# Optimization experiments

Hardware: AMD Instinct MI355X
Metric: run time of the kernel (lower is better)

The kernel has to match this reference:

```python
import jax, jax.numpy as jnp
import numpy as np

N, E, D = 20000, 160000, 128   # nodes, edges, d_model
GH, HC = 4, 128                # TransformerConv heads, per-head channels (= out_channels)
MH = 4                         # temporal MHA heads
MC = D // MH                   # temporal MHA per-head dim
EPS = 1e-5


def layer_norm(x, g, b):
    mu = x.mean(-1, keepdims=True)
    var = ((x - mu) ** 2).mean(-1, keepdims=True)
    return (x - mu) * jax.lax.rsqrt(var + EPS) * g + b


def forward(x, temporal_encoding, gq_w, gq_b, gk_w, gk_b, gv_w, gv_b, gs_w, gs_b,
            mha_wq, mha_bq, mha_wk, mha_bk, mha_wv, mha_bv, mha_wo, mha_bo,
            ffn_w1, ffn_b1, ffn_w2, ffn_b2,
            ln1_g, ln1_b, ln2_g, ln2_b, ln3_g, ln3_b, edge_index):
    src, dst = edge_index[0], edge_index[1]
    n = x.shape[0]
    # --- TransformerConv(in=D, out=D, heads=GH, concat=False, root_weight=True) ---
    q = (x @ gq_w.T + gq_b).reshape(n, GH, HC)
    k = (x @ gk_w.T + gk_b).reshape(n, GH, HC)
    v = (x @ gv_w.T + gv_b).reshape(n, GH, HC)
    # per-edge attention logits: <q_i, k_j> / sqrt(out_channels), message j->i
    alpha = (q[dst] * k[src]).sum(-1) / jnp.sqrt(jnp.asarray(HC, x.dtype))  # [E, GH]
    # numerically-stable segment softmax over incoming edges of each dst node
    m = jax.ops.segment_max(alpha, dst, num_segments=n)                     # [N, GH]
    ex = jnp.exp(alpha - m[dst])
    den = jax.ops.segment_sum(ex, dst, num_segments=n)
    w = ex / den[dst]                                                       # [E, GH]
    agg = jax.ops.segment_sum(w[..., None] * v[src], dst, num_segments=n)  # [N, GH, HC]
    graph_out = agg.mean(1) + (x @ gs_w.T + gs_b)  # concat=False -> head mean; + root skip lin
    x1 = layer_norm(x + graph_out, ln1_g, ln1_b)   # dropout is identity at eval
    # --- temporal MHA: per-node query (len 1) attends to its temporal encoding (kv len 1) ---
    tq = (x1 @ mha_wq.T + mha_bq).reshape(n, MH, MC)
    tk = (temporal_encoding @ mha_wk.T + mha_bk).reshape(n, MH, MC)
    tv = (temporal_encoding @ mha_wv.T + mha_bv).reshape(n, MH, MC)
    scores = (tq * tk).sum(-1, keepdims=True) / jnp.sqrt(jnp.asarray(MC, x.dtype))  # [N, MH, 1]
    attn = jax.nn.softmax(scores, axis=-1)  # exactly ones (single kv position); kept for fidelity
    temp_out = (attn * tv).reshape(n, D) @ mha_wo.T + mha_bo
    x2 = layer_norm(x1 + temp_out, ln2_g, ln2_b)
    # --- FFN ---
    h = jax.nn.relu(x2 @ ffn_w1.T + ffn_b1)
    ffn_out = h @ ffn_w2.T + ffn_b2
    return layer_norm(x2 + ffn_out, ln3_g, ln3_b)


def setup_inputs() -> dict:
    ks = jax.random.split(jax.random.key(0), 16)
    s = 0.05
    def p(i, shape):
        return jax.random.normal(ks[i], shape, jnp.float32) * s
    z = lambda *sh: jnp.zeros(sh, jnp.float32)
    o = lambda *sh: jnp.ones(sh, jnp.float32)
    return {
        "x": p(0, (N, D)),
        "temporal_encoding": p(1, (N, D)),
        "gq_w": p(2, (GH * HC, D)), "gq_b": z(GH * HC),
        "gk_w": p(3, (GH * HC, D)), "gk_b": z(GH * HC),
        "gv_w": p(4, (GH * HC, D)), "gv_b": z(GH * HC),
        "gs_w": p(5, (D, D)), "gs_b": z(D),
        "mha_wq": p(6, (D, D)), "mha_bq": z(D),
        "mha_wk": p(7, (D, D)), "mha_bk": z(D),
        "mha_wv": p(8, (D, D)), "mha_bv": z(D),
        "mha_wo": p(9, (D, D)), "mha_bo": z(D),
        "ffn_w1": p(10, (4 * D, D)), "ffn_b1": z(4 * D),
        "ffn_w2": p(11, (D, 4 * D)), "ffn_b2": z(D),
        "ln1_g": o(D), "ln1_b": z(D),
        "ln2_g": o(D), "ln2_b": z(D),
        "ln3_g": o(D), "ln3_b": z(D),
        "edge_index": jax.random.randint(ks[12], (2, E), 0, N, jnp.int32),
    }


def reference(x, temporal_encoding, gq_w, gq_b, gk_w, gk_b, gv_w, gv_b, gs_w, gs_b,
              mha_wq, mha_bq, mha_wk, mha_bk, mha_wv, mha_bv, mha_wo, mha_bo,
              ffn_w1, ffn_b1, ffn_w2, ffn_b2,
              ln1_g, ln1_b, ln2_g, ln2_b, ln3_g, ln3_b, edge_index):
    return forward(x, temporal_encoding, gq_w, gq_b, gk_w, gk_b, gv_w, gv_b, gs_w, gs_b,
                   mha_wq, mha_bq, mha_wk, mha_bk, mha_wv, mha_bv, mha_wo, mha_bo,
                   ffn_w1, ffn_b1, ffn_w2, ffn_b2,
                   ln1_g, ln1_b, ln2_g, ln2_b, ln3_g, ln3_b, edge_index)
```

## Files before the change

### kernel.cpp

```cpp
#include <hip/hip_runtime.h>

#define NN 20000
#define EE 160000
#define DD 128
#define GHC 512
#define INV_SQRT_HC 0.08838834764831845f

typedef __attribute__((ext_vector_type(8))) short short8;
typedef __attribute__((ext_vector_type(4))) short short4v;
typedef __attribute__((ext_vector_type(4))) float float4v;
typedef __attribute__((ext_vector_type(2))) float float2v;
typedef __attribute__((ext_vector_type(4))) unsigned uint4v;
typedef __attribute__((ext_vector_type(2))) unsigned uint2v;

__device__ inline float bf2f(unsigned short u) {
    union { unsigned u; float f; } x; x.u = ((unsigned)u) << 16; return x.f;
}
__device__ inline unsigned short f2bf(float f) {
    union { float f; unsigned u; } x; x.f = f;
    unsigned u = x.u;
    unsigned r = (u + 0x7fffu + ((u >> 16) & 1u)) >> 16;
    return (unsigned short)r;
}

#if defined(__has_builtin)
#if __has_builtin(__builtin_amdgcn_cvt_pk_f32_fp8) && __has_builtin(__builtin_amdgcn_cvt_pk_fp8_f32)
#define HW_FP8 1
#endif
#endif
#ifndef HW_FP8
#define HW_FP8 0
#endif

#if !HW_FP8
__device__ inline unsigned char sw_enc_fp8(float f) {
    if (!(f == f)) return 0x7f;
    unsigned s = (f < 0.f) ? 0x80u : 0u;
    float a = fabsf(f);
    if (a >= 448.f) return (unsigned char)(s | 0x7e);
    if (a < 5.96046448e-8f) return (unsigned char)s;
    int e; frexpf(a, &e);
    int E = e - 1;
    if (E < -6) E = -6;
    float q = ldexpf(rintf(ldexpf(a, 3 - E)), E - 3);
    if (q == 0.f) return (unsigned char)s;
    union { float f; unsigned u; } x; x.f = q;
    int qe = (int)((x.u >> 23) & 0xff) - 127;
    if (qe < -6) {
        unsigned mant = (unsigned)rintf(ldexpf(q, 9));
        return (unsigned char)(s | mant);
    }
    unsigned mant = (x.u >> 20) & 7;
    int ebits = qe + 7;
    if (ebits > 15) { ebits = 15; mant = 6; }
    return (unsigned char)(s | ((unsigned)ebits << 3) | mant);
}
__device__ inline float sw_dec_fp8(unsigned char u) {
    unsigned s = u >> 7, e = (u >> 3) & 15, m = u & 7;
    float v = e ? ldexpf((float)(8 + m), (int)e - 10) : ldexpf((float)m, -9);
    return s ? -v : v;
}
#endif

__device__ inline unsigned short fp8_enc2(float a, float b) {
#if HW_FP8
    int r = __builtin_amdgcn_cvt_pk_fp8_f32(a, b, 0, false);
    return (unsigned short)(r & 0xffff);
#else
    return (unsigned short)(sw_enc_fp8(a) | ((unsigned)sw_enc_fp8(b) << 8));
#endif
}
__device__ inline float2v fp8_dec2_lo(unsigned w) {
#if HW_FP8
    return __builtin_amdgcn_cvt_pk_f32_fp8((int)w, false);
#else
    float2v r;
    r[0] = sw_dec_fp8((unsigned char)(w & 0xff));
    r[1] = sw_dec_fp8((unsigned char)((w >> 8) & 0xff));
    return r;
#endif
}
__device__ inline float2v fp8_dec2_hi(unsigned w) {
#if HW_FP8
    return __builtin_amdgcn_cvt_pk_f32_fp8((int)w, true);
#else
    float2v r;
    r[0] = sw_dec_fp8((unsigned char)((w >> 16) & 0xff));
    r[1] = sw_dec_fp8((unsigned char)(w >> 24));
    return r;
#endif
}

struct WPack { const void* in[18]; };
__device__ __constant__ const int WSZ[18] = {
    65536, 65536, 65536, 512, 512, 512,
    16384, 128, 65536, 512, 65536, 128,
    128, 128, 128, 128, 128, 128 };

__global__ void prep_kernel(const float* __restrict__ x, const float* __restrict__ te,
                            unsigned short* __restrict__ xcout, WPack p,
                            unsigned short* __restrict__ wcout,
                            const float* __restrict__ wv, const float* __restrict__ bv,
                            const float* __restrict__ wo, const float* __restrict__ bo,
                            unsigned short* __restrict__ wcomb,
                            unsigned short* __restrict__ bcomb,
                            const int* __restrict__ e_dst, int* __restrict__ counts)
{
    const int b = blockIdx.x;
    const int tid = threadIdx.x;
    if (b < 1024) {
        const long n4half = (long)NN * DD / 4;
        short4v* out4 = reinterpret_cast<short4v*>(xcout);
        long i = (long)b * 256 + tid;
        const long stride = 1024L * 256;
        const long tot = 2 * n4half;
        for (; i < tot; i += stride) {
            const float4v* src = (i < n4half)
                ? reinterpret_cast<const float4v*>(x)
                : reinterpret_cast<const float4v*>(te) - n4half;
            float4v v = src[i];
            short4v o;
            o[0] = (short)f2bf(v[0]); o[1] = (short)f2bf(v[1]);
            o[2] = (short)f2bf(v[2]); o[3] = (short)f2bf(v[3]);
            out4[i] = o;
        }
    } else if (b < 1600) {
        const int seg = (b - 1024) >> 5;
        const int rep = (b - 1024) & 31;
        int off = 0;
#pragma unroll
        for (int s = 0; s < 18; ++s) if (s < seg) off += WSZ[s];
        const int n = WSZ[seg];
        const float* q = (const float*)p.in[seg];
        for (int i = rep * 256 + tid; i < n; i += 32 * 256)
            wcout[off + i] = f2bf(q[i]);
    } else if (b < 1664) {
        int e = (b - 1600) * 256 + tid;
        int i = e >> 7, kk = e & 127;
        float s = 0.f;
        for (int j = 0; j < 128; ++j)
            s += wo[i * 128 + j] * wv[j * 128 + kk];
        wcomb[e] = f2bf(s);
        if (b == 1600 && tid < 128) {
            float t = 0.f;
            for (int j = 0; j < 128; ++j) t += wo[tid * 128 + j] * bv[j];
            bcomb[tid] = f2bf(t + bo[tid]);
        }
    } else {
        int e = (b - 1664) * 256 + tid;
        if (e < EE) {
            int d = e_dst[e];
            if (d >= 0 && d < NN) atomicAdd(&counts[d], 1);
        }
    }
}

__global__ __launch_bounds__(256) void gemm3_kernel(
    const unsigned short* __restrict__ A, const unsigned short* __restrict__ W,
    const unsigned short* __restrict__ bias, unsigned short* __restrict__ out,
    unsigned char* __restrict__ kvout, int M, int Nout, int split, int relu,
    int nxg, int ncol)
{
    __shared__ short8 wslab[2048];
    __shared__ __attribute__((aligned(16))) unsigned stile[4][16][36];
    const int tid  = threadIdx.x;
    const int lane = tid & 63;
    const int wid  = tid >> 6;
    const int quad = lane >> 4;
    const int l15  = lane & 15;

    const int nb  = nxg * ncol;
    const int qq  = nb >> 3, rm = nb & 7;
    const int xcd = blockIdx.x & 7, slot = blockIdx.x >> 3;
    const int c   = (xcd < rm) ? xcd * (qq + 1) + slot
                               : rm * (qq + 1) + (xcd - rm) * qq + slot;
    const int xg = c / ncol;
    const int yg = c - xg * ncol;
    const int colbase0 = yg * 128;
    const int rowg = xg * 256;

    const bool isfp8 = (colbase0 >= split);
    const int kvcol = colbase0 - split;
    const int which = isfp8 ? (kvcol >> 9) : 0;
    const int head  = isfp8 ? ((kvcol & 511) >> 7) : 0;

    const short8* A8 = reinterpret_cast<const short8*>(A);
    const short8* W8 = reinterpret_cast<const short8*>(W);

    short8 a4[4];
    {
        int arow = rowg + wid * 16 + l15;
        if (arow >= M) arow = M - 1;
#pragma unroll
        for (int i = 0; i < 4; ++i) a4[i] = A8[(size_t)arow * 16 + i * 4 + quad];
    }

#pragma unroll
    for (int rep = 0; rep < 8; ++rep) {
        int f   = rep * 256 + tid;
        int fl  = f & 63;
        int fi  = (f >> 6) & 3;
        int ft  = (f >> 8) & 3;
        int ftt = f >> 10;
        int wrow = colbase0 + ftt * 64 + 16 * ft + (fl & 15);
        wslab[f] = W8[(size_t)wrow * 16 + fi * 4 + (fl >> 4)];
    }

    float bvv[2][4];
#pragma unroll
    for (int tt = 0; tt < 2; ++tt)
#pragma unroll
        for (int t = 0; t < 4; ++t)
            bvv[tt][t] = bf2f(bias[colbase0 + tt * 64 + 16 * t + l15]);

    __syncthreads();

    unsigned short* fp = reinterpret_cast<unsigned short*>(&stile[wid][0][0]);

#pragma unroll
    for (int tg = 0; tg < 4; ++tg) {
        const int rowbase = rowg + tg * 64 + wid * 16;

        short8 a4n[4];
        if (tg < 3) {
            int arow = rowbase + 64 + l15;
            if (arow >= M) arow = M - 1;
#pragma unroll
            for (int i = 0; i < 4; ++i) a4n[i] = A8[(size_t)arow * 16 + i * 4 + quad];
        }

#pragma unroll
        for (int tt = 0; tt < 2; ++tt) {
            float4v acc[4];
#pragma unroll
            for (int t = 0; t < 4; ++t) acc[t] = (float4v){0.f, 0.f, 0.f, 0.f};

#pragma unroll
            for (int i = 0; i < 4; ++i) {
#pragma unroll
                for (int t = 0; t < 4; ++t) {
                    short8 b = wslab[((tt * 4 + t) * 4 + i) * 64 + lane];
                    acc[t] = __builtin_amdgcn_mfma_f32_16x16x32_bf16(a4[i], b, acc[t], 0, 0, 0);
                }
            }

            if (!isfp8) {
#pragma unroll
                for (int t = 0; t < 4; ++t) {
#pragma unroll
                    for (int r = 0; r < 4; ++r) {
                        float vv = acc[t][r] + bvv[tt][t];
                        if (relu) vv = fmaxf(vv, 0.f);
                        float ov = __shfl_xor(vv, 1, 64);
                        if ((l15 & 1) == 0)
                            stile[wid][quad * 4 + r][8 * t + (l15 >> 1)] =
                                (unsigned)f2bf(vv) | ((unsigned)f2bf(ov) << 16);
                    }
                }
                const int rr0 = lane >> 3;
                const int cd  = (lane & 7) * 4;
#pragma unroll
                for (int it = 0; it < 2; ++it) {
                    int rw = rr0 + it * 8;
                    int grow = rowbase + rw;
                    if (grow < M) {
                        uint4v v = *reinterpret_cast<const uint4v*>(&stile[wid][rw][cd]);
                        *reinterpret_cast<uint4v*>(&out[(size_t)grow * Nout + colbase0 + tt * 64 + cd * 2]) = v;
                    }
                }
            } else {
#pragma unroll
                for (int t = 0; t < 4; ++t) {
#pragma unroll
                    for (int r = 0; r < 4; ++r) {
                        float vv = (acc[t][r] + bvv[tt][t]) * 256.f;
                        float ov = __shfl_xor(vv, 1, 64);
                        if ((l15 & 1) == 0)
                            fp[(quad * 4 + r) * 72 + tt * 32 + ((16 * t + l15) >> 1)] =
                                fp8_enc2(vv, ov);
                    }
                }
            }
        }

        if (isfp8) {
#pragma unroll
            for (int it = 0; it < 2; ++it) {
                int u = lane + it * 64;
                int row = u >> 3;
                int part = u & 7;
                int grow = rowbase + row;
                if (grow < M) {
                    uint4v v = *reinterpret_cast<const uint4v*>(&fp[row * 72 + part * 8]);
                    size_t ro = (size_t)grow * 1024 + (size_t)which * 512
                              + (size_t)head * 128 + (size_t)part * 16;
                    *reinterpret_cast<uint4v*>(kvout + ro) = v;
                }
            }
        }

        if (tg < 3) {
#pragma unroll
            for (int i = 0; i < 4; ++i) a4[i] = a4n[i];
        }
    }
}

__global__ __launch_bounds__(256) void gemm_ln2_kernel(
    const unsigned short* __restrict__ A, const unsigned short* __restrict__ W,
    const unsigned short* __restrict__ bias,
    const float* __restrict__ residf, const float* __restrict__ c,
    const unsigned short* __restrict__ g, const unsigned short* __restrict__ beta,
    float* __restrict__ outf, unsigned short* __restrict__ outb, int M, int K)
{
    __shared__ short8 wslab[2048];
    __shared__ unsigned short stile[4][16][136];
    const int tid  = threadIdx.x;
    const int lane = tid & 63;
    const int wid  = tid >> 6;
    const int quad = lane >> 4;
    const int l15  = lane & 15;
    const int rowbase = blockIdx.x * 64 + wid * 16;

    int arow = rowbase + l15;
    if (arow >= M) arow = M - 1;

    const short8* A8 = reinterpret_cast<const short8*>(A);
    const short8* W8 = reinterpret_cast<const short8*>(W);
    const int k8 = K >> 3;
    const int kchunks = K >> 7;

    float4v acc[2][4];
#pragma unroll
    for (int tt = 0; tt < 2; ++tt)
#pragma unroll
        for (int t = 0; t < 4; ++t) acc[tt][t] = (float4v){0.f, 0.f, 0.f, 0.f};

    for (int cc = 0; cc < kchunks; ++cc) {
        if (cc > 0) __syncthreads();
#pragma unroll
        for (int rep = 0; rep < 8; ++rep) {
            int f   = rep * 256 + tid;
            int fl  = f & 63;
            int fi  = (f >> 6) & 3;
            int ft  = (f >> 8) & 3;
            int ftt = f >> 10;
            int wrow = ftt * 64 + 16 * ft + (fl & 15);
            wslab[f] = W8[(size_t)wrow * k8 + cc * 16 + fi * 4 + (fl >> 4)];
        }
        short8 a4[4];
#pragma unroll
        for (int i = 0; i < 4; ++i) a4[i] = A8[(size_t)arow * k8 + cc * 16 + i * 4 + quad];
        __syncthreads();
#pragma unroll
        for (int tt = 0; tt < 2; ++tt)
#pragma unroll
            for (int i = 0; i < 4; ++i)
#pragma unroll
                for (int t = 0; t < 4; ++t) {
                    short8 b = wslab[((tt * 4 + t) * 4 + i) * 64 + lane];
                    acc[tt][t] = __builtin_amdgcn_mfma_f32_16x16x32_bf16(a4[i], b, acc[tt][t], 0, 0, 0);
                }
    }

#pragma unroll
    for (int tt = 0; tt < 2; ++tt)
#pragma unroll
        for (int t = 0; t < 4; ++t) {
            float bv = bf2f(bias[tt * 64 + 16 * t + l15]);
#pragma unroll
            for (int r = 0; r < 4; ++r)
                stile[wid][quad * 4 + r][tt * 64 + 16 * t + l15] = f2bf(acc[tt][t][r] + bv);
        }

    const int r  = lane >> 2;
    const int p  = lane & 3;
    const int grow = rowbase + r;
    const int gr = (grow < M) ? grow : M - 1;

    float v[32];
    const short8* st8 = reinterpret_cast<const short8*>(&stile[wid][r][p * 32]);
#pragma unroll
    for (int q = 0; q < 4; ++q) {
        short8 sb = st8[q];
#pragma unroll
        for (int j = 0; j < 8; ++j) v[q * 8 + j] = bf2f((unsigned short)sb[j]);
    }
    const float4v* r4 = reinterpret_cast<const float4v*>(&residf[(size_t)gr * 128 + p * 32]);
#pragma unroll
    for (int q = 0; q < 8; ++q) {
        float4v rv = r4[q];
#pragma unroll
        for (int j = 0; j < 4; ++j) v[q * 4 + j] += rv[j];
    }
    if (c) {
        const float4v* c4 = reinterpret_cast<const float4v*>(&c[(size_t)gr * 128 + p * 32]);
#pragma unroll
        for (int q = 0; q < 8; ++q) {
            float4v cv = c4[q];
#pragma unroll
            for (int j = 0; j < 4; ++j) v[q * 4 + j] += cv[j];
        }
    }
    float s = 0.f, sq = 0.f;
#pragma unroll
    for (int i = 0; i < 32; ++i) { s += v[i]; sq += v[i] * v[i]; }
    s  += __shfl_xor(s, 1, 64);  s  += __shfl_xor(s, 2, 64);
    sq += __shfl_xor(sq, 1, 64); sq += __shfl_xor(sq, 2, 64);
    float mu  = s * (1.f / 128.f);
    float var = sq * (1.f / 128.f) - mu * mu;
    float rs  = rsqrtf(fmaxf(var, 0.f) + 1e-5f);

    if (grow < M) {
        const short8* g8 = reinterpret_cast<const short8*>(&g[p * 32]);
        const short8* b8 = reinterpret_cast<const short8*>(&beta[p * 32]);
        float o[32];
#pragma unroll
        for (int q = 0; q < 4; ++q) {
            short8 gg = g8[q], bb = b8[q];
#pragma unroll
            for (int j = 0; j < 8; ++j)
                o[q * 8 + j] = (v[q * 8 + j] - mu) * rs * bf2f((unsigned short)gg[j])
                               + bf2f((unsigned short)bb[j]);
        }
        float4v* o4 = reinterpret_cast<float4v*>(outf + (size_t)grow * 128 + p * 32);
#pragma unroll
        for (int q = 0; q < 8; ++q) {
            float4v ov = {o[q * 4], o[q * 4 + 1], o[q * 4 + 2], o[q * 4 + 3]};
            o4[q] = ov;
        }
        if (outb) {
            short8* ob8 = reinterpret_cast<short8*>(outb + (size_t)grow * 128 + p * 32);
#pragma unroll
            for (int q = 0; q < 4; ++q) {
                short8 oo;
#pragma unroll
                for (int j = 0; j < 8; ++j) oo[j] = (short)f2bf(o[q * 8 + j]);
                ob8[q] = oo;
            }
        }
    }
}

__global__ __launch_bounds__(1024) void scan_kernel(
    const int* __restrict__ counts, int* __restrict__ offsets, int* __restrict__ pos, int n)
{
    __shared__ int wsum[16];
    __shared__ int carry_s;
    const int tid = threadIdx.x;
    const int wid = tid >> 6, lane = tid & 63;
    int vals[20];
#pragma unroll
    for (int cI = 0; cI < 20; ++cI) {
        int i = cI * 1024 + tid;
        vals[cI] = (i < n) ? counts[i] : 0;
    }
    if (tid == 0) carry_s = 0;
    __syncthreads();
#pragma unroll
    for (int cI = 0; cI < 20; ++cI) {
        int i = cI * 1024 + tid;
        int val = vals[cI];
        int x = val;
#pragma unroll
        for (int off = 1; off < 64; off <<= 1) {
            int t = __shfl_up(x, off, 64);
            if (lane >= off) x += t;
        }
        if (lane == 63) wsum[wid] = x;
        __syncthreads();
        if (wid == 0 && lane < 16) {
            int s = wsum[lane];
#pragma unroll
            for (int off = 1; off < 16; off <<= 1) {
                int t = __shfl_up(s, off, 64);
                if (lane >= off) s += t;
            }
            wsum[lane] = s;
        }
        __syncthreads();
        int prefix = (wid > 0 ? wsum[wid - 1] : 0) + carry_s;
        int ex = prefix + x - val;
        if (i < n) { offsets[i] = ex; pos[i] = ex; }
        __syncthreads();
        if (tid == 0) carry_s += wsum[15];
        __syncthreads();
    }
    if (tid == 0) offsets[n] = carry_s;
}

__global__ void scatter_kernel(const int* __restrict__ src, const int* __restrict__ dst,
                               int* __restrict__ pos, int* __restrict__ sorted_src, int E)
{
    int e = blockIdx.x * 256 + threadIdx.x;
    if (e < E) {
        int d = dst[e];
        if (d >= 0 && d < NN) {
            int p = atomicAdd(&pos[d], 1);
            if (p >= 0 && p < E) sorted_src[p] = src[e];
        }
    }
}

__device__ inline void agg_edge(const uint2v& kk, const uint2v& vv,
                                const float* qf, float* acc, float& ssum)
{
    float2v k01 = fp8_dec2_lo(kk[0]);
    float2v k23 = fp8_dec2_hi(kk[0]);
    float2v k45 = fp8_dec2_lo(kk[1]);
    float2v k67 = fp8_dec2_hi(kk[1]);
    float dot = qf[0] * k01[0] + qf[1] * k01[1] + qf[2] * k23[0] + qf[3] * k23[1]
              + qf[4] * k45[0] + qf[5] * k45[1] + qf[6] * k67[0] + qf[7] * k67[1];
    dot += __shfl_xor(dot, 1, 64);
    dot += __shfl_xor(dot, 2, 64);
    dot += __shfl_xor(dot, 4, 64);
    dot += __shfl_xor(dot, 8, 64);
    float pp = __expf(dot);
    ssum += pp;
    float2v v01 = fp8_dec2_lo(vv[0]);
    float2v v23 = fp8_dec2_hi(vv[0]);
    float2v v45 = fp8_dec2_lo(vv[1]);
    float2v v67 = fp8_dec2_hi(vv[1]);
    acc[0] += pp * v01[0]; acc[1] += pp * v01[1];
    acc[2] += pp * v23[0]; acc[3] += pp * v23[1];
    acc[4] += pp * v45[0]; acc[5] += pp * v45[1];
    acc[6] += pp * v67[0]; acc[7] += pp * v67[1];
}

__global__ __launch_bounds__(256) void agg_kernel(
    const unsigned short* __restrict__ q, const unsigned char* __restrict__ kvb,
    const int* __restrict__ offsets, const int* __restrict__ srcs,
    float* __restrict__ aggb)
{
    __shared__ float sacc[4][64][8];
    __shared__ float sssum[4][64];
    const int tid  = threadIdx.x;
    const int wid  = tid >> 6;
    const int lane = tid & 63;
    const int node = blockIdx.x * 2 + (wid >> 1);
    const int half = wid & 1;

    const short8* q8 = reinterpret_cast<const short8*>(q);
    const int fidx = (lane >> 4) * 16 + (lane & 15);
    const int koff = fidx * 8;

    short8 qv = q8[(size_t)node * 64 + fidx];
    float qf[8];
#pragma unroll
    for (int i = 0; i < 8; ++i)
        qf[i] = bf2f((unsigned short)qv[i]) * (INV_SQRT_HC / 256.f);

    int beg = offsets[node], end = offsets[node + 1];
    if (beg < 0) beg = 0;
    if (end > EE) end = EE;
    float ssum = 0.f;
    float acc[8];
#pragma unroll
    for (int i = 0; i < 8; ++i) acc[i] = 0.f;

    const int start = beg + half;
    int nce = (end > start) ? ((end - start + 1) >> 1) : 0;
    int ncap = (nce > 64) ? 64 : nce;

    int sv = 0;
    if (lane < ncap) {
        int s = srcs[start + 2 * lane];
        if (s < 0) s = 0;
        if (s >= NN) s = NN - 1;
        sv = s;
    }
    if (ncap > 0) {
        int s0 = __shfl(sv, 0, 64);
        uint2v kc = *reinterpret_cast<const uint2v*>(kvb + (size_t)s0 * 1024 + koff);
        uint2v vc = *reinterpret_cast<const uint2v*>(kvb + (size_t)s0 * 1024 + 512 + koff);
        for (int i = 0; i < ncap; ++i) {
            uint2v kn, vn;
            if (i + 1 < ncap) {
                int sn = __shfl(sv, i + 1, 64);
                kn = *reinterpret_cast<const uint2v*>(kvb + (size_t)sn * 1024 + koff);
                vn = *reinterpret_cast<const uint2v*>(kvb + (size_t)sn * 1024 + 512 + koff);
            }
            agg_edge(kc, vc, qf, acc, ssum);
            kc = kn; vc = vn;
        }
    }
    for (int j = start + 128; j < end; j += 2) {
        int s = srcs[j];
        if (s < 0) s = 0;
        if (s >= NN) s = NN - 1;
        uint2v kc = *reinterpret_cast<const uint2v*>(kvb + (size_t)s * 1024 + koff);
        uint2v vc = *reinterpret_cast<const uint2v*>(kvb + (size_t)s * 1024 + 512 + koff);
        agg_edge(kc, vc, qf, acc, ssum);
    }

#pragma unroll
    for (int i = 0; i < 8; ++i) sacc[wid][lane][i] = acc[i];
    sssum[wid][lane] = ssum;
    __syncthreads();
    if (half == 0) {
#pragma unroll
        for (int i = 0; i < 8; ++i) acc[i] += sacc[wid ^ 1][lane][i];
        ssum += sssum[wid ^ 1][lane];

        float inv = (ssum > 0.f) ? 1.f / (256.f * ssum) : 0.f;
#pragma unroll
        for (int i = 0; i < 8; ++i) acc[i] *= inv;
#pragma unroll
        for (int i = 0; i < 8; ++i) {
            acc[i] += __shfl_xor(acc[i], 16, 64);
            acc[i] += __shfl_xor(acc[i], 32, 64);
            acc[i] *= 0.25f;
        }
        if (lane < 16) {
            float4v* o = reinterpret_cast<float4v*>(aggb + (size_t)node * 128 + lane * 8);
            o[0] = (float4v){acc[0], acc[1], acc[2], acc[3]};
            o[1] = (float4v){acc[4], acc[5], acc[6], acc[7]};
        }
    }
}

extern "C" void kernel_launch(void* const* d_in, const int* in_sizes, int n_in,
                              void* d_out, int out_size, void* d_ws, size_t ws_size,
                              hipStream_t stream)
{
    const int* edge_index = (const int*)d_in[28];
    const int* e_src = edge_index;
    const int* e_dst = edge_index + EE;

    if (n_in < 29 || in_sizes[0] != NN * DD || in_sizes[28] != 2 * EE || out_size != NN * DD)
        return;

    const size_t SZ_OFF  = (size_t)(NN + 16) * 4;
    const size_t SZ_CNT  = (size_t)NN * 4;
    const size_t SZ_SS   = (size_t)EE * 4;
    const size_t SZ_SM   = (size_t)NN * DD * 2;
    const size_t SZ_F32  = (size_t)NN * DD * 4;
    const size_t SZ_Q    = (size_t)NN * 512 * 2;
    const size_t SZ_KV   = (size_t)NN * 1024;
    const size_t SZ_HB   = (size_t)NN * GHC * 2;
    const size_t WC_ELE  = 347136;
    const size_t SZ_WC   = WC_ELE * 2;
    const size_t SZ_WCB  = 16384 * 2 + 256;
    const size_t REQUIRED = SZ_OFF + 2 * SZ_CNT + SZ_SS + 2 * SZ_SM + SZ_WC + SZ_WCB
                          + SZ_Q + SZ_KV + 3 * SZ_F32 + SZ_SM + SZ_HB;

    if (ws_size < REQUIRED) return;

    char* w = (char*)d_ws;
    int* offsets = (int*)w;        w += SZ_OFF;
    int* counts  = (int*)w;        w += SZ_CNT;
    int* pos     = (int*)w;        w += SZ_CNT;
    int* sorted_src = (int*)w;     w += SZ_SS;
    unsigned short* xc   = (unsigned short*)w; w += SZ_SM;
    unsigned short* tec  = (unsigned short*)w; w += SZ_SM;
    unsigned short* wc   = (unsigned short*)w; w += SZ_WC;
    unsigned short* wcomb = (unsigned short*)w; w += 16384 * 2;
    unsigned short* bcomb = (unsigned short*)w; w += 256;
    unsigned short* qb   = (unsigned short*)w; w += SZ_Q;
    unsigned char*  kvb  = (unsigned char*)w;  w += SZ_KV;
    float*          aggb = (float*)w;          w += SZ_F32;
    float*          x1f  = (float*)w;          w += SZ_F32;
    float*          x2f  = (float*)w;          w += SZ_F32;
    unsigned short* x2b  = (unsigned short*)w; w += SZ_SM;
    unsigned short* hbuf = (unsigned short*)w; w += SZ_HB;

    unsigned short* cw = wc;
    unsigned short* qkv_w = cw; cw += 3 * 65536;
    unsigned short* qkv_b = cw; cw += 3 * 512;
    unsigned short* gs_w  = cw; cw += 16384;  unsigned short* gs_b  = cw; cw += 128;
    unsigned short* ffn_w1 = cw; cw += 65536; unsigned short* ffn_b1 = cw; cw += 512;
    unsigned short* ffn_w2 = cw; cw += 65536; unsigned short* ffn_b2 = cw; cw += 128;
    unsigned short* ln1_g = cw; cw += 128;    unsigned short* ln1_b = cw; cw += 128;
    unsigned short* ln2_g = cw; cw += 128;    unsigned short* ln2_b = cw; cw += 128;
    unsigned short* ln3_g = cw; cw += 128;    unsigned short* ln3_b = cw; cw += 128;

    const int EB = (EE + 255) / 256;
    const dim3 blk(256);
    const int MB = (NN + 63) / 64;
    const int MB2 = (NN + 255) / 256;

    WPack pack;
    const int live_idx[18] = {2,4,6, 3,5,7, 8,9, 18,19, 20,21, 22,23,24,25,26,27};
    for (int i = 0; i < 18; ++i) pack.in[i] = d_in[live_idx[i]];

    (void)hipMemsetAsync(counts, 0, SZ_CNT, stream);
    prep_kernel<<<1664 + EB, blk, 0, stream>>>((const float*)d_in[0], (const float*)d_in[1],
                                               xc, pack, wc,
                                               (const float*)d_in[14], (const float*)d_in[15],
                                               (const float*)d_in[16], (const float*)d_in[17],
                                               wcomb, bcomb, e_dst, counts);

    scan_kernel<<<1, 1024, 0, stream>>>(counts, offsets, pos, NN);
    scatter_kernel<<<EB, blk, 0, stream>>>(e_src, e_dst, pos, sorted_src, EE);

    gemm3_kernel<<<dim3(MB2 * 12), blk, 0, stream>>>(xc, qkv_w, qkv_b, qb, kvb,
                                                     NN, 512, 512, 0, MB2, 12);
    agg_kernel<<<NN / 2, blk, 0, stream>>>(qb, kvb, offsets, sorted_src, aggb);
    gemm_ln2_kernel<<<MB, blk, 0, stream>>>(xc, gs_w, gs_b, (const float*)d_in[0], aggb,
                                            ln1_g, ln1_b, x1f, nullptr, NN, DD);
    gemm_ln2_kernel<<<MB, blk, 0, stream>>>(tec, wcomb, bcomb, x1f, nullptr,
                                            ln2_g, ln2_b, x2f, x2b, NN, DD);
    gemm3_kernel<<<dim3(MB2 * 4), blk, 0, stream>>>(x2b, ffn_w1, ffn_b1, hbuf, nullptr,
                                                    NN, 512, 99999, 1, MB2, 4);
    gemm_ln2_kernel<<<MB, blk, 0, stream>>>(hbuf, ffn_w2, ffn_b2, x2f, nullptr,
                                            ln3_g, ln3_b, (float*)d_out, nullptr, NN, GHC);
}
```

Measured before the change: 289.1 us.

## Fuse LN1 and temporal-attention LN2 GEMMs; use direct-to-LDS weight loads and swizzled staging

Merges the two back-to-back GEMM+LayerNorm kernels into one kernel. x1 stays in registers between the graph-skip GEMM+LN1 and the temporal combined-weight GEMM+LN2, so the fp32 x1 round trip through global memory and one launch go away. Weight slabs in the GEMM kernels are now staged with global_load_lds direct-to-LDS copies instead of going through registers. The output staging tiles use XOR swizzling in place of padding to avoid LDS bank conflicts. The fused kernel reloads the LDS weight slab mid-kernel and uses more registers, which may reduce occupancy.

Measured after the change: 288.0 us. Within noise of the previous version (-0.4%).

```diff
diff --git a/kernel.cpp b/kernel.cpp
--- a/kernel.cpp
+++ b/kernel.cpp
@@ -21,6 +21,12 @@
     unsigned u = x.u;
     unsigned r = (u + 0x7fffu + ((u >> 16) & 1u)) >> 16;
     return (unsigned short)r;
+}
+
+__device__ inline void stage16(const short8* gsrc, short8* ldst) {
+    __builtin_amdgcn_global_load_lds(
+        (const __attribute__((address_space(1))) void*)gsrc,
+        (__attribute__((address_space(3))) void*)ldst, 16, 0, 0);
 }
 
 #if defined(__has_builtin)
@@ -162,7 +168,7 @@
     int nxg, int ncol)
 {
     __shared__ short8 wslab[2048];
-    __shared__ __attribute__((aligned(16))) unsigned stile[4][16][36];
+    __shared__ __attribute__((aligned(16))) unsigned stile4[4][16][32];
     const int tid  = threadIdx.x;
     const int lane = tid & 63;
     const int wid  = tid >> 6;
@@ -197,13 +203,11 @@
 
 #pragma unroll
     for (int rep = 0; rep < 8; ++rep) {
-        int f   = rep * 256 + tid;
-        int fl  = f & 63;
-        int fi  = (f >> 6) & 3;
-        int ft  = (f >> 8) & 3;
-        int ftt = f >> 10;
-        int wrow = colbase0 + ftt * 64 + 16 * ft + (fl & 15);
-        wslab[f] = W8[(size_t)wrow * 16 + fi * 4 + (fl >> 4)];
+        const int fi  = (rep * 4 + wid) & 3;
+        const int ft  = rep & 3;
+        const int ftt = rep >> 2;
+        const int wrow = colbase0 + ftt * 64 + 16 * ft + l15;
+        stage16(&W8[(size_t)wrow * 16 + fi * 4 + quad], &wslab[rep * 256 + wid * 64]);
     }
 
     float bvv[2][4];
@@ -215,7 +219,7 @@
 
     __syncthreads();
 
-    unsigned short* fp = reinterpret_cast<unsigned short*>(&stile[wid][0][0]);
+    unsigned short* fp = reinterpret_cast<unsigned short*>(&stile4[wid][0][0]);
 
 #pragma unroll
     for (int tg = 0; tg < 4; ++tg) {
@@ -252,9 +256,12 @@
                         float vv = acc[t][r] + bvv[tt][t];
                         if (relu) vv = fmaxf(vv, 0.f);
                         float ov = __shfl_xor(vv, 1, 64);
-                        if ((l15 & 1) == 0)
-                            stile[wid][quad * 4 + r][8 * t + (l15 >> 1)] =
+                        if ((l15 & 1) == 0) {
+                            const int row = quad * 4 + r;
+                            const int cs  = (8 * t + (l15 >> 1)) ^ ((row & 7) << 2);
+                            stile4[wid][row][cs] =
                                 (unsigned)f2bf(vv) | ((unsigned)f2bf(ov) << 16);
+                        }
                     }
                 }
                 const int rr0 = lane >> 3;
@@ -264,7 +271,8 @@
                     int rw = rr0 + it * 8;
                     int grow = rowbase + rw;
                     if (grow < M) {
-                        uint4v v = *reinterpret_cast<const uint4v*>(&stile[wid][rw][cd]);
+                        const int cs = cd ^ ((rw & 7) << 2);
+                        uint4v v = *reinterpret_cast<const uint4v*>(&stile4[wid][rw][cs]);
                         *reinterpret_cast<uint4v*>(&out[(size_t)grow * Nout + colbase0 + tt * 64 + cd * 2]) = v;
                     }
                 }
@@ -275,9 +283,11 @@
                     for (int r = 0; r < 4; ++r) {
                         float vv = (acc[t][r] + bvv[tt][t]) * 256.f;
                         float ov = __shfl_xor(vv, 1, 64);
-                        if ((l15 & 1) == 0)
-                            fp[(quad * 4 + r) * 72 + tt * 32 + ((16 * t + l15) >> 1)] =
-                                fp8_enc2(vv, ov);
+                        if ((l15 & 1) == 0) {
+                            const int row = quad * 4 + r;
+                            const int u = row * 64 + tt * 32 + 8 * t + (l15 >> 1);
+                            fp[u ^ ((row & 7) << 3)] = fp8_enc2(vv, ov);
+                        }
                     }
                 }
             }
@@ -291,7 +301,8 @@
                 int part = u & 7;
                 int grow = rowbase + row;
                 if (grow < M) {
-                    uint4v v = *reinterpret_cast<const uint4v*>(&fp[row * 72 + part * 8]);
+                    const int ui = (row * 64 + part * 8) ^ ((row & 7) << 3);
+                    uint4v v = *reinterpret_cast<const uint4v*>(&fp[ui]);
                     size_t ro = (size_t)grow * 1024 + (size_t)which * 512
                               + (size_t)head * 128 + (size_t)part * 16;
                     *reinterpret_cast<uint4v*>(kvout + ro) = v;
@@ -340,13 +351,12 @@
         if (cc > 0) __syncthreads();
 #pragma unroll
         for (int rep = 0; rep < 8; ++rep) {
-            int f   = rep * 256 + tid;
-            int fl  = f & 63;
-            int fi  = (f >> 6) & 3;
-            int ft  = (f >> 8) & 3;
-            int ftt = f >> 10;
-            int wrow = ftt * 64 + 16 * ft + (fl & 15);
-            wslab[f] = W8[(size_t)wrow * k8 + cc * 16 + fi * 4 + (fl >> 4)];
+            const int fi  = (rep * 4 + wid) & 3;
+            const int ft  = rep & 3;
+            const int ftt = rep >> 2;
+            const int wrow = ftt * 64 + 16 * ft + l15;
+            stage16(&W8[(size_t)wrow * k8 + cc * 16 + fi * 4 + quad],
+                    &wslab[rep * 256 + wid * 64]);
         }
         short8 a4[4];
 #pragma unroll
@@ -438,6 +448,204 @@
                 for (int j = 0; j < 8; ++j) oo[j] = (short)f2bf(o[q * 8 + j]);
                 ob8[q] = oo;
             }
+        }
+    }
+}
+
+__global__ __launch_bounds__(256) void gemm_ln12_kernel(
+    const unsigned short* __restrict__ A1, const unsigned short* __restrict__ W1,
+    const unsigned short* __restrict__ b1,
+    const float* __restrict__ rx, const float* __restrict__ ragg,
+    const unsigned short* __restrict__ g1, const unsigned short* __restrict__ be1,
+    const unsigned short* __restrict__ A2, const unsigned short* __restrict__ W2,
+    const unsigned short* __restrict__ b2,
+    const unsigned short* __restrict__ g2, const unsigned short* __restrict__ be2,
+    float* __restrict__ outf, unsigned short* __restrict__ outb, int M)
+{
+    __shared__ short8 wslab[2048];
+    __shared__ unsigned short stile[4][16][136];
+    const int tid  = threadIdx.x;
+    const int lane = tid & 63;
+    const int wid  = tid >> 6;
+    const int quad = lane >> 4;
+    const int l15  = lane & 15;
+    const int rowbase = blockIdx.x * 64 + wid * 16;
+
+    int arow = rowbase + l15;
+    if (arow >= M) arow = M - 1;
+
+    const short8* A81 = reinterpret_cast<const short8*>(A1);
+    const short8* A82 = reinterpret_cast<const short8*>(A2);
+    const short8* W81 = reinterpret_cast<const short8*>(W1);
+    const short8* W82 = reinterpret_cast<const short8*>(W2);
+
+#pragma unroll
+    for (int rep = 0; rep < 8; ++rep) {
+        const int fi  = (rep * 4 + wid) & 3;
+        const int ft  = rep & 3;
+        const int ftt = rep >> 2;
+        const int wrow = ftt * 64 + 16 * ft + l15;
+        stage16(&W81[(size_t)wrow * 16 + fi * 4 + quad], &wslab[rep * 256 + wid * 64]);
+    }
+    short8 a4[4];
+#pragma unroll
+    for (int i = 0; i < 4; ++i) a4[i] = A81[(size_t)arow * 16 + i * 4 + quad];
+    __syncthreads();
+
+    float4v acc1[2][4];
+#pragma unroll
+    for (int tt = 0; tt < 2; ++tt)
+#pragma unroll
+        for (int t = 0; t < 4; ++t) acc1[tt][t] = (float4v){0.f, 0.f, 0.f, 0.f};
+#pragma unroll
+    for (int tt = 0; tt < 2; ++tt)
+#pragma unroll
+        for (int i = 0; i < 4; ++i)
+#pragma unroll
+            for (int t = 0; t < 4; ++t) {
+                short8 b = wslab[((tt * 4 + t) * 4 + i) * 64 + lane];
+                acc1[tt][t] = __builtin_amdgcn_mfma_f32_16x16x32_bf16(a4[i], b, acc1[tt][t], 0, 0, 0);
+            }
+    __syncthreads();
+
+#pragma unroll
+    for (int rep = 0; rep < 8; ++rep) {
+        const int fi  = (rep * 4 + wid) & 3;
+        const int ft  = rep & 3;
+        const int ftt = rep >> 2;
+        const int wrow = ftt * 64 + 16 * ft + l15;
+        stage16(&W82[(size_t)wrow * 16 + fi * 4 + quad], &wslab[rep * 256 + wid * 64]);
+    }
+    short8 a42[4];
+#pragma unroll
+    for (int i = 0; i < 4; ++i) a42[i] = A82[(size_t)arow * 16 + i * 4 + quad];
+
+#pragma unroll
+    for (int tt = 0; tt < 2; ++tt)
+#pragma unroll
+        for (int t = 0; t < 4; ++t) {
+            float bv = bf2f(b1[tt * 64 + 16 * t + l15]);
+#pragma unroll
+            for (int r = 0; r < 4; ++r)
+                stile[wid][quad * 4 + r][tt * 64 + 16 * t + l15] = f2bf(acc1[tt][t][r] + bv);
+        }
+
+    const int r  = lane >> 2;
+    const int p  = lane & 3;
+    const int grow = rowbase + r;
+    const int gr = (grow < M) ? grow : M - 1;
+
+    float v[32];
+    {
+        const short8* st8 = reinterpret_cast<const short8*>(&stile[wid][r][p * 32]);
+#pragma unroll
+        for (int q = 0; q < 4; ++q) {
+            short8 sb = st8[q];
+#pragma unroll
+            for (int j = 0; j < 8; ++j) v[q * 8 + j] = bf2f((unsigned short)sb[j]);
+        }
+        const float4v* r4 = reinterpret_cast<const float4v*>(&rx[(size_t)gr * 128 + p * 32]);
+        const float4v* c4 = reinterpret_cast<const float4v*>(&ragg[(size_t)gr * 128 + p * 32]);
+#pragma unroll
+        for (int q = 0; q < 8; ++q) {
+            float4v rv = r4[q];
+            float4v cv = c4[q];
+#pragma unroll
+            for (int j = 0; j < 4; ++j) v[q * 4 + j] += rv[j] + cv[j];
+        }
+    }
+    float x1[32];
+    {
+        float s = 0.f, sq = 0.f;
+#pragma unroll
+        for (int i = 0; i < 32; ++i) { s += v[i]; sq += v[i] * v[i]; }
+        s  += __shfl_xor(s, 1, 64);  s  += __shfl_xor(s, 2, 64);
+        sq += __shfl_xor(sq, 1, 64); sq += __shfl_xor(sq, 2, 64);
+        float mu  = s * (1.f / 128.f);
+        float var = sq * (1.f / 128.f) - mu * mu;
+        float rs  = rsqrtf(fmaxf(var, 0.f) + 1e-5f);
+        const short8* g8 = reinterpret_cast<const short8*>(&g1[p * 32]);
+        const short8* b8 = reinterpret_cast<const short8*>(&be1[p * 32]);
+#pragma unroll
+        for (int q = 0; q < 4; ++q) {
+            short8 gg = g8[q], bb = b8[q];
+#pragma unroll
+            for (int j = 0; j < 8; ++j)
+                x1[q * 8 + j] = (v[q * 8 + j] - mu) * rs * bf2f((unsigned short)gg[j])
+                                + bf2f((unsigned short)bb[j]);
+        }
+    }
+
+    __syncthreads();
+
+    float4v acc2[2][4];
+#pragma unroll
+    for (int tt = 0; tt < 2; ++tt)
+#pragma unroll
+        for (int t = 0; t < 4; ++t) acc2[tt][t] = (float4v){0.f, 0.f, 0.f, 0.f};
+#pragma unroll
+    for (int tt = 0; tt < 2; ++tt)
+#pragma unroll
+        for (int i = 0; i < 4; ++i)
+#pragma unroll
+            for (int t = 0; t < 4; ++t) {
+                short8 b = wslab[((tt * 4 + t) * 4 + i) * 64 + lane];
+                acc2[tt][t] = __builtin_amdgcn_mfma_f32_16x16x32_bf16(a42[i], b, acc2[tt][t], 0, 0, 0);
+            }
+
+#pragma unroll
+    for (int tt = 0; tt < 2; ++tt)
+#pragma unroll
+        for (int t = 0; t < 4; ++t) {
+            float bv = bf2f(b2[tt * 64 + 16 * t + l15]);
+#pragma unroll
+            for (int r2 = 0; r2 < 4; ++r2)
+                stile[wid][quad * 4 + r2][tt * 64 + 16 * t + l15] = f2bf(acc2[tt][t][r2] + bv);
+        }
+
+    {
+        const short8* st8 = reinterpret_cast<const short8*>(&stile[wid][r][p * 32]);
+#pragma unroll
+        for (int q = 0; q < 4; ++q) {
+            short8 sb = st8[q];
+#pragma unroll
+            for (int j = 0; j < 8; ++j) v[q * 8 + j] = bf2f((unsigned short)sb[j]) + x1[q * 8 + j];
+        }
+    }
+    float s = 0.f, sq = 0.f;
+#pragma unroll
+    for (int i = 0; i < 32; ++i) { s += v[i]; sq += v[i] * v[i]; }
+    s  += __shfl_xor(s, 1, 64);  s  += __shfl_xor(s, 2, 64);
+    sq += __shfl_xor(sq, 1, 64); sq += __shfl_xor(sq, 2, 64);
+    float mu  = s * (1.f / 128.f);
+    float var = sq * (1.f / 128.f) - mu * mu;
+    float rs  = rsqrtf(fmaxf(var, 0.f) + 1e-5f);
+
+    if (grow < M) {
+        const short8* g8 = reinterpret_cast<const short8*>(&g2[p * 32]);
+        const short8* b8 = reinterpret_cast<const short8*>(&be2[p * 32]);
+        float o[32];
+#pragma unroll
+        for (int q = 0; q < 4; ++q) {
+            short8 gg = g8[q], bb = b8[q];
+#pragma unroll
+            for (int j = 0; j < 8; ++j)
+                o[q * 8 + j] = (v[q * 8 + j] - mu) * rs * bf2f((unsigned short)gg[j])
+                               + bf2f((unsigned short)bb[j]);
+        }
+        float4v* o4 = reinterpret_cast<float4v*>(outf + (size_t)grow * 128 + p * 32);
+#pragma unroll
+        for (int q = 0; q < 8; ++q) {
+            float4v ov = {o[q * 4], o[q * 4 + 1], o[q * 4 + 2], o[q * 4 + 3]};
+            o4[q] = ov;
+        }
+        short8* ob8 = reinterpret_cast<short8*>(outb + (size_t)grow * 128 + p * 32);
+#pragma unroll
+        for (int q = 0; q < 4; ++q) {
+            short8 oo;
+#pragma unroll
+            for (int j = 0; j < 8; ++j) oo[j] = (short)f2bf(o[q * 8 + j]);
+            ob8[q] = oo;
         }
     }
 }
@@ -663,6 +871,7 @@
     float*          x2f  = (float*)w;          w += SZ_F32;
     unsigned short* x2b  = (unsigned short*)w; w += SZ_SM;
     unsigned short* hbuf = (unsigned short*)w; w += SZ_HB;
+    (void)x1f;
 
     unsigned short* cw = wc;
     unsigned short* qkv_w = cw; cw += 3 * 65536;
@@ -696,10 +905,11 @@
     gemm3_kernel<<<dim3(MB2 * 12), blk, 0, stream>>>(xc, qkv_w, qkv_b, qb, kvb,
                                                      NN, 512, 512, 0, MB2, 12);
     agg_kernel<<<NN / 2, blk, 0, stream>>>(qb, kvb, offsets, sorted_src, aggb);
-    gemm_ln2_kernel<<<MB, blk, 0, stream>>>(xc, gs_w, gs_b, (const float*)d_in[0], aggb,
-                                            ln1_g, ln1_b, x1f, nullptr, NN, DD);
-    gemm_ln2_kernel<<<MB, blk, 0, stream>>>(tec, wcomb, bcomb, x1f, nullptr,
-                                            ln2_g, ln2_b, x2f, x2b, NN, DD);
+    gemm_ln12_kernel<<<MB, blk, 0, stream>>>(xc, gs_w, gs_b,
+                                             (const float*)d_in[0], aggb,
+                                             ln1_g, ln1_b,
+                                             tec, wcomb, bcomb,
+                                             ln2_g, ln2_b, x2f, x2b, NN);
     gemm3_kernel<<<dim3(MB2 * 4), blk, 0, stream>>>(x2b, ffn_w1, ffn_b1, hbuf, nullptr,
                                                     NN, 512, 99999, 1, MB2, 4);
     gemm_ln2_kernel<<<MB, blk, 0, stream>>>(hbuf, ffn_w2, ffn_b2, x2f, nullptr,
```
